# Performance work log

Measured on AMD Instinct MI355X. Metric: run time of the kernel, lower is better.

The kernel has to match this reference:

```python
import jax, jax.numpy as jnp
import numpy as np

EMBED = 768
HEADS = 12
HEAD_DIM = EMBED // HEADS
HIDDEN = 4 * EMBED


def layer_norm(x, gamma, beta, eps=1e-5):
    mu = jnp.mean(x, axis=-1, keepdims=True)
    var = jnp.var(x, axis=-1, keepdims=True)
    return (x - mu) * jax.lax.rsqrt(var + eps) * gamma + beta


def setup_inputs() -> dict:
    key = jax.random.key(0)
    ks = jax.random.split(key, 10)
    B, N, C = 64, 577, EMBED
    s_in = 1.0 / np.sqrt(C)
    s_hid = 1.0 / np.sqrt(HIDDEN)
    return {
        "x": jax.random.normal(ks[0], (B, N, C), jnp.float32),
        "ln1_g": jnp.ones((C,), jnp.float32),
        "ln1_b": jnp.zeros((C,), jnp.float32),
        "w_qkv": jax.random.normal(ks[1], (C, 3 * C), jnp.float32) * s_in,  # no bias (qkv_bias=False)
        "w_proj": jax.random.normal(ks[2], (C, C), jnp.float32) * s_in,
        "b_proj": jnp.zeros((C,), jnp.float32),
        "ln2_g": jnp.ones((C,), jnp.float32),
        "ln2_b": jnp.zeros((C,), jnp.float32),
        "w_fc1": jax.random.normal(ks[3], (C, HIDDEN), jnp.float32) * s_in,
        "b_fc1": jnp.zeros((HIDDEN,), jnp.float32),
        "w_fc2": jax.random.normal(ks[4], (HIDDEN, C), jnp.float32) * s_hid,
        "b_fc2": jnp.zeros((C,), jnp.float32),
    }


def reference(x, ln1_g, ln1_b, w_qkv, w_proj, b_proj, ln2_g, ln2_b, w_fc1, b_fc1, w_fc2, b_fc2):
    B, N, C = x.shape
    # --- attention branch (pre-norm) ---
    h = layer_norm(x, ln1_g, ln1_b)
    qkv = (h @ w_qkv).reshape(B, N, 3, HEADS, HEAD_DIM)
    q = jnp.transpose(qkv[:, :, 0], (0, 2, 1, 3))  # [B,H,N,D]
    k = jnp.transpose(qkv[:, :, 1], (0, 2, 1, 3))
    v = jnp.transpose(qkv[:, :, 2], (0, 2, 1, 3))
    scale = HEAD_DIM ** -0.5
    att = jax.nn.softmax(jnp.einsum("bhnd,bhmd->bhnm", q, k) * scale, axis=-1)
    o = jnp.einsum("bhnm,bhmd->bhnd", att, v)
    o = jnp.transpose(o, (0, 2, 1, 3)).reshape(B, N, C)
    x = x + (o @ w_proj + b_proj)
    # --- MLP branch (pre-norm) ---
    h = layer_norm(x, ln2_g, ln2_b)
    h = jax.nn.gelu(h @ w_fc1 + b_fc1, approximate=False)
    x = x + (h @ w_fc2 + b_fc2)
    return x
```

## Files before the change

kernel.cpp:

```cpp
#include <hip/hip_runtime.h>
#include <hip/hip_bf16.h>
#include <math.h>

using bf16 = __hip_bfloat16;
typedef __attribute__((ext_vector_type(8))) short short8;
typedef __attribute__((ext_vector_type(4))) float f32x4;

#define NSEQ   577
#define NBATCH 64
#define NTOK   36928
#define MPAD   37120
#define NHEADS 12
#define HDIM   64
#define NP     640
#define CEMB   768
#define CHID   3072
#define NBH    (NBATCH*NHEADS)

__device__ __forceinline__ bf16 f2bf(float v){ return __float2bfloat16(v); }

__device__ __forceinline__ float gelu_f(float x) {
    float x3 = x * x * x;
    float y = 1.5957691216057308f * (x + 0.044715f * x3);
    float e = __expf(y);
    float t = 1.0f - 2.0f / (e + 1.0f);
    return 0.5f * x * (1.0f + t);
}

#define GLOAD_LDS16(gaddr, laddr) \
  __builtin_amdgcn_global_load_lds((__attribute__((address_space(1))) const void*)(gaddr), \
                                   (__attribute__((address_space(3))) void*)(laddr), 16, 0, 0)

__global__ __launch_bounds__(256) void transpose_w(const float* __restrict__ src,
                                                   bf16* __restrict__ dst, int R, int C) {
    long idx = (long)blockIdx.x * 256 + threadIdx.x;
    long total = (long)R * C;
    if (idx < total) {
        int r = (int)(idx / C);
        int c = (int)(idx - (long)r * C);
        dst[(long)c * R + r] = f2bf(src[idx]);
    }
}

__global__ __launch_bounds__(256) void ln_kernel(const float* __restrict__ x,
                                                 const float* __restrict__ gamma,
                                                 const float* __restrict__ beta,
                                                 bf16* __restrict__ out) {
    int row = blockIdx.x;
    const float* xr = x + (size_t)row * CEMB;
    int tid = threadIdx.x;
    float v0 = xr[tid], v1 = xr[tid + 256], v2 = xr[tid + 512];
    float s = v0 + v1 + v2;
    #pragma unroll
    for (int o = 32; o > 0; o >>= 1) s += __shfl_down(s, o);
    __shared__ float red[4];
    if ((tid & 63) == 0) red[tid >> 6] = s;
    __syncthreads();
    float mean = (red[0] + red[1] + red[2] + red[3]) * (1.0f / CEMB);
    float d0 = v0 - mean, d1 = v1 - mean, d2 = v2 - mean;
    float q = d0*d0 + d1*d1 + d2*d2;
    #pragma unroll
    for (int o = 32; o > 0; o >>= 1) q += __shfl_down(q, o);
    __shared__ float red2[4];
    if ((tid & 63) == 0) red2[tid >> 6] = q;
    __syncthreads();
    float var = (red2[0] + red2[1] + red2[2] + red2[3]) * (1.0f / CEMB);
    float rs = rsqrtf(var + 1e-5f);
    bf16* orow = out + (size_t)row * CEMB;
    orow[tid]       = f2bf(d0 * rs * gamma[tid]       + beta[tid]);
    orow[tid + 256] = f2bf(d1 * rs * gamma[tid + 256] + beta[tid + 256]);
    orow[tid + 512] = f2bf(d2 * rs * gamma[tid + 512] + beta[tid + 512]);
}

__global__ __launch_bounds__(256) void flash_attn(const bf16* __restrict__ qg,
                                                  const bf16* __restrict__ kg,
                                                  const bf16* __restrict__ vtg,
                                                  bf16* __restrict__ og) {
    const int tid = threadIdx.x, lane = tid & 63, w = tid >> 6;
    const int fr = lane & 15, fh = lane >> 4;
    const int bh = blockIdx.y;
    const int q0 = blockIdx.x * 128;
    const int wr = w * 32;

    __shared__ bf16 Ks[2][64 * 64];
    __shared__ bf16 Vs[2][64 * 64];
    __shared__ bf16 Ps[128 * 64];

    const bf16* qb = qg  + (size_t)bh * NP * HDIM;
    const bf16* kb = kg  + (size_t)bh * NP * HDIM;
    const bf16* vb = vtg + (size_t)bh * HDIM * NP;

    const int swz  = (fr & 7) << 3;
    const int scol = (((lane & 7) ^ (lane >> 3)) << 3);
    const int srow = lane >> 3;

    short8 qa[2][2];
    #pragma unroll
    for (int mi = 0; mi < 2; mi++)
        #pragma unroll
        for (int ks = 0; ks < 2; ks++)
            qa[mi][ks] = *reinterpret_cast<const short8*>(
                qb + (size_t)(q0 + wr + mi * 16 + fr) * HDIM + ks * 32 + fh * 8);
    #pragma unroll
    for (int mi = 0; mi < 2; mi++)
        #pragma unroll
        for (int ks = 0; ks < 2; ks++)
            asm volatile("" : "+v"(qa[mi][ks]));

    f32x4 od[2][4] = {};
    float m_run[2][4], l_run[2][4];
    #pragma unroll
    for (int mi = 0; mi < 2; mi++)
        #pragma unroll
        for (int r = 0; r < 4; r++) { m_run[mi][r] = -1e30f; l_run[mi][r] = 0.f; }

    auto stageKV = [&](int buf, int kb0) {
        GLOAD_LDS16(kb + (size_t)(kb0 + w * 8 + srow) * HDIM + scol,      Ks[buf] + w * 512);
        GLOAD_LDS16(kb + (size_t)(kb0 + 32 + w * 8 + srow) * HDIM + scol, Ks[buf] + 2048 + w * 512);
        GLOAD_LDS16(vb + (size_t)(w * 8 + srow) * NP + kb0 + scol,        Vs[buf] + w * 512);
        GLOAD_LDS16(vb + (size_t)(32 + w * 8 + srow) * NP + kb0 + scol,   Vs[buf] + 2048 + w * 512);
    };

    auto tileBody = [&](int buf, int kb0) {
        f32x4 sacc[2][4] = {};
        short8 kf[4][2];
        #pragma unroll
        for (int n = 0; n < 4; n++)
            #pragma unroll
            for (int ks = 0; ks < 2; ks++)
                kf[n][ks] = *reinterpret_cast<const short8*>(
                    &Ks[buf][(n * 16 + fr) * 64 + ((ks * 32 + fh * 8) ^ swz)]);
        __builtin_amdgcn_s_setprio(1);
        #pragma unroll
        for (int mi = 0; mi < 2; mi++)
            #pragma unroll
            for (int n = 0; n < 4; n++)
                #pragma unroll
                for (int ks = 0; ks < 2; ks++)
                    sacc[mi][n] = __builtin_amdgcn_mfma_f32_16x16x32_bf16(qa[mi][ks], kf[n][ks], sacc[mi][n], 0, 0, 0);
        __builtin_amdgcn_s_setprio(0);

        #pragma unroll
        for (int mi = 0; mi < 2; mi++) {
            float sv[4][4];
            float tm[4] = {-1e30f, -1e30f, -1e30f, -1e30f};
            #pragma unroll
            for (int n = 0; n < 4; n++) {
                int col = kb0 + n * 16 + fr;
                bool valid = col < NSEQ;
                #pragma unroll
                for (int r = 0; r < 4; r++) {
                    float s = sacc[mi][n][r];
                    sv[n][r] = valid ? s : -1e30f;
                    tm[r] = fmaxf(tm[r], sv[n][r]);
                }
            }
            #pragma unroll
            for (int r = 0; r < 4; r++) {
                #pragma unroll
                for (int o = 1; o < 16; o <<= 1) tm[r] = fmaxf(tm[r], __shfl_xor(tm[r], o));
                float mo = m_run[mi][r];
                if (tm[r] - mo > 8.f) {
                    float sc = __expf(mo - tm[r]);
                    mo = tm[r];
                    m_run[mi][r] = mo;
                    l_run[mi][r] *= sc;
                    #pragma unroll
                    for (int n2 = 0; n2 < 4; n2++) od[mi][n2][r] *= sc;
                }
                float ps = 0.f;
                #pragma unroll
                for (int n = 0; n < 4; n++) {
                    float e = __expf(sv[n][r] - mo);
                    sv[n][r] = e; ps += e;
                }
                #pragma unroll
                for (int o = 1; o < 16; o <<= 1) ps += __shfl_xor(ps, o);
                l_run[mi][r] += ps;
            }
            #pragma unroll
            for (int n = 0; n < 4; n++)
                #pragma unroll
                for (int r = 0; r < 4; r++)
                    Ps[(wr + mi * 16 + fh * 4 + r) * 64 +
                       ((n * 16 + fr) ^ (((fh * 4 + r) & 7) << 3))] = f2bf(sv[n][r]);
        }
        asm volatile("s_waitcnt lgkmcnt(0)" ::: "memory");
        __builtin_amdgcn_sched_barrier(0);

        short8 pa[2][2], vf[4][2];
        #pragma unroll
        for (int mi = 0; mi < 2; mi++)
            #pragma unroll
            for (int ks = 0; ks < 2; ks++)
                pa[mi][ks] = *reinterpret_cast<const short8*>(
                    &Ps[(wr + mi * 16 + fr) * 64 + ((ks * 32 + fh * 8) ^ swz)]);
        #pragma unroll
        for (int n2 = 0; n2 < 4; n2++)
            #pragma unroll
            for (int ks = 0; ks < 2; ks++)
                vf[n2][ks] = *reinterpret_cast<const short8*>(
                    &Vs[buf][(n2 * 16 + fr) * 64 + ((ks * 32 + fh * 8) ^ swz)]);
        __builtin_amdgcn_s_setprio(1);
        #pragma unroll
        for (int mi = 0; mi < 2; mi++)
            #pragma unroll
            for (int n2 = 0; n2 < 4; n2++)
                #pragma unroll
                for (int ks = 0; ks < 2; ks++)
                    od[mi][n2] = __builtin_amdgcn_mfma_f32_16x16x32_bf16(pa[mi][ks], vf[n2][ks], od[mi][n2], 0, 0, 0);
        __builtin_amdgcn_s_setprio(0);
    };

    stageKV(0, 0);
    stageKV(1, 64);
    for (int t = 0; t < 9; ++t) {
        asm volatile("s_waitcnt vmcnt(4)" ::: "memory");
        __builtin_amdgcn_s_barrier();
        tileBody(t & 1, t * 64);
        asm volatile("s_waitcnt lgkmcnt(0)" ::: "memory");
        __builtin_amdgcn_s_barrier();
        if (t + 2 < 10) stageKV(t & 1, (t + 2) * 64);
    }
    asm volatile("s_waitcnt vmcnt(0)" ::: "memory");
    __builtin_amdgcn_s_barrier();
    tileBody(1, 9 * 64);

    const int b = bh / NHEADS, hh = bh - b * NHEADS;
    #pragma unroll
    for (int mi = 0; mi < 2; mi++)
        #pragma unroll
        for (int r = 0; r < 4; r++) {
            int qrow = q0 + wr + mi * 16 + fh * 4 + r;
            if (qrow < NSEQ) {
                float inv = 1.f / l_run[mi][r];
                #pragma unroll
                for (int n2 = 0; n2 < 4; n2++)
                    og[((size_t)(b * NSEQ + qrow)) * CEMB + hh * HDIM + n2 * 16 + fr] =
                        f2bf(od[mi][n2][r] * inv);
            }
        }
}

#define MODE_QKV  1
#define MODE_PROJ 3
#define MODE_FC1  4
#define MODE_FC2  5

struct GemmParams {
    const bf16* A;
    const bf16* Bt;
    int M, N, K;
    int Mreal;
    float* Cf;
    bf16* Cb;
    const float* bias;
    const float* resid;
    bf16* qb; bf16* kb; bf16* vtb;
};

template<int MODE>
__global__ __launch_bounds__(512, 2) void gemm256(GemmParams p) {
    __shared__ bf16 AsBuf[2][256 * 64];
    __shared__ bf16 BsBuf[2][256 * 64];
    const int tid  = threadIdx.x;
    const int lane = tid & 63;
    const int w    = tid >> 6;

    const int gx = gridDim.x, gy = gridDim.y;
    const int nwg = gx * gy;
    const int orig = blockIdx.y * gx + blockIdx.x;
    const int q8 = nwg >> 3, r8 = nwg & 7;
    const int xcd = orig & 7, oid = orig >> 3;
    const int lin2 = ((xcd < r8) ? xcd * (q8 + 1) : r8 * (q8 + 1) + (xcd - r8) * q8) + oid;
    const int bm = (lin2 / gy) * 256;
    const int bn = (lin2 % gy) * 256;

    const int Kd = p.K;
    const int wm = w >> 2, wn = w & 3;
    const int wr = wm * 128, wc = wn * 64;
    const int fr = lane & 15;
    const int fk = (lane >> 4) * 8;
    const int swz = (fr & 7) << 3;

    const int sr = w * 8 + (lane >> 3);
    const int scol = (((lane & 7) ^ (lane >> 3)) << 3);
    const bf16* aS[4]; const bf16* bS[4];
    #pragma unroll
    for (int s = 0; s < 4; s++) {
        aS[s] = p.A  + (size_t)(bm + s * 64 + sr) * Kd + scol;
        bS[s] = p.Bt + (size_t)(bn + s * 64 + sr) * Kd + scol;
    }

    f32x4 acc[8][4] = {};

    auto stage = [&](bf16* Ad, bf16* Bd) {
        #pragma unroll
        for (int s = 0; s < 4; s++) {
            GLOAD_LDS16(aS[s], Ad + (size_t)(s * 8 + w) * 512);
            GLOAD_LDS16(bS[s], Bd + (size_t)(s * 8 + w) * 512);
            aS[s] += 64; bS[s] += 64;
        }
    };
    auto compute = [&](const bf16* Ad, const bf16* Bd) {
        #pragma unroll
        for (int ks = 0; ks < 2; ks++) {
            short8 b[4];
            #pragma unroll
            for (int n = 0; n < 4; n++)
                b[n] = *reinterpret_cast<const short8*>(
                    &Bd[(wc + n * 16 + fr) * 64 + ((ks * 32 + fk) ^ swz)]);
            #pragma unroll
            for (int m = 0; m < 8; m++) {
                short8 a = *reinterpret_cast<const short8*>(
                    &Ad[(wr + m * 16 + fr) * 64 + ((ks * 32 + fk) ^ swz)]);
                #pragma unroll
                for (int n = 0; n < 4; n++)
                    acc[m][n] = __builtin_amdgcn_mfma_f32_16x16x32_bf16(a, b[n], acc[m][n], 0, 0, 0);
            }
        }
    };

    const int T = Kd >> 6;
    stage(AsBuf[0], BsBuf[0]);
    stage(AsBuf[1], BsBuf[1]);
    for (int t = 0; t < T - 1; ++t) {
        asm volatile("s_waitcnt vmcnt(8)" ::: "memory");
        __builtin_amdgcn_s_barrier();
        compute(AsBuf[t & 1], BsBuf[t & 1]);
        asm volatile("s_waitcnt lgkmcnt(0)" ::: "memory");
        __builtin_amdgcn_s_barrier();
        if (t + 2 < T) stage(AsBuf[t & 1], BsBuf[t & 1]);
    }
    asm volatile("s_waitcnt vmcnt(0)" ::: "memory");
    __builtin_amdgcn_s_barrier();
    compute(AsBuf[(T - 1) & 1], BsBuf[(T - 1) & 1]);

    const int fq = (lane >> 4) * 4;
    const int colw = bn + wc;

    if (MODE == MODE_QKV) {
        const int which = colw / CEMB;
        const int hh = (colw - which * CEMB) >> 6;
        const float scl = (which == 0) ? 0.125f : 1.0f;
        #pragma unroll
        for (int m = 0; m < 8; m++)
        #pragma unroll
        for (int r = 0; r < 4; r++) {
            int row = bm + wr + m * 16 + fq + r;
            if (row < p.Mreal) {
                int b2 = row / NSEQ;
                int n2 = row - b2 * NSEQ;
                size_t bh = (size_t)b2 * NHEADS + hh;
                if (which == 0) {
                    bf16* dst = p.qb + (bh * NP + n2) * HDIM + fr;
                    #pragma unroll
                    for (int n = 0; n < 4; n++) dst[n * 16] = f2bf(acc[m][n][r] * scl);
                } else if (which == 1) {
                    bf16* dst = p.kb + (bh * NP + n2) * HDIM + fr;
                    #pragma unroll
                    for (int n = 0; n < 4; n++) dst[n * 16] = f2bf(acc[m][n][r]);
                } else {
                    bf16* dst = p.vtb + (bh * HDIM + fr) * NP + n2;
                    #pragma unroll
                    for (int n = 0; n < 4; n++) dst[(size_t)n * 16 * NP] = f2bf(acc[m][n][r]);
                }
            }
        }
    } else if (MODE == MODE_FC1) {
        const float* bp = p.bias + colw + fr;
        float bb[4];
        #pragma unroll
        for (int n = 0; n < 4; n++) bb[n] = bp[n * 16];
        #pragma unroll
        for (int m = 0; m < 8; m++)
        #pragma unroll
        for (int r = 0; r < 4; r++) {
            int row = bm + wr + m * 16 + fq + r;
            if (row < p.Mreal) {
                bf16* crow = p.Cb + (size_t)row * p.N + colw + fr;
                #pragma unroll
                for (int n = 0; n < 4; n++)
                    crow[n * 16] = f2bf(gelu_f(acc[m][n][r] + bb[n]));
            }
        }
    } else {
        const float* bp = p.bias + colw + fr;
        float bb[4];
        #pragma unroll
        for (int n = 0; n < 4; n++) bb[n] = bp[n * 16];
        #pragma unroll
        for (int m = 0; m < 8; m++)
        #pragma unroll
        for (int r = 0; r < 4; r++) {
            int row = bm + wr + m * 16 + fq + r;
            if (row < p.Mreal) {
                float* crow = p.Cf + (size_t)row * p.N + colw + fr;
                const float* rrow = p.resid + (size_t)row * p.N + colw + fr;
                #pragma unroll
                for (int n = 0; n < 4; n++)
                    crow[n * 16] = acc[m][n][r] + bb[n] + rrow[n * 16];
            }
        }
    }
}

extern "C" void kernel_launch(void* const* d_in, const int* in_sizes, int n_in,
                              void* d_out, int out_size, void* d_ws, size_t ws_size,
                              hipStream_t stream) {
    const float* x      = (const float*)d_in[0];
    const float* ln1_g  = (const float*)d_in[1];
    const float* ln1_b  = (const float*)d_in[2];
    const float* w_qkv  = (const float*)d_in[3];
    const float* w_proj = (const float*)d_in[4];
    const float* b_proj = (const float*)d_in[5];
    const float* ln2_g  = (const float*)d_in[6];
    const float* ln2_b  = (const float*)d_in[7];
    const float* w_fc1  = (const float*)d_in[8];
    const float* b_fc1  = (const float*)d_in[9];
    const float* w_fc2  = (const float*)d_in[10];
    const float* b_fc2  = (const float*)d_in[11];
    float* out = (float*)d_out;

    char* ws = (char*)d_ws;
    auto al = [](size_t b){ return (b + 255) & ~(size_t)255; };
    size_t off = 0;
    auto take = [&](size_t b)->char* { char* p = ws + off; off += al(b); return p; };

    bf16* wqkvT  = (bf16*)take((size_t)2304 * 768 * 2);
    bf16* wprojT = (bf16*)take((size_t)768 * 768 * 2);
    bf16* wfc1T  = (bf16*)take((size_t)3072 * 768 * 2);
    bf16* wfc2T  = (bf16*)take((size_t)768 * 3072 * 2);
    bf16* h      = (bf16*)take((size_t)MPAD * CEMB * 2);
    bf16* o      = (bf16*)take((size_t)MPAD * CEMB * 2);
    size_t fixedEnd = off;

    const size_t qkvB = (size_t)NBH * NP * HDIM * 2;
    bf16* q_c  = (bf16*)(ws + fixedEnd);
    bf16* k_c  = (bf16*)(ws + fixedEnd + qkvB);
    bf16* vT_c = (bf16*)(ws + fixedEnd + 2 * qkvB);
    bf16* g_c  = (bf16*)(ws + fixedEnd);

    transpose_w<<<(768 * 2304 + 255) / 256, 256, 0, stream>>>(w_qkv, wqkvT, 768, 2304);
    transpose_w<<<(768 * 768 + 255) / 256, 256, 0, stream>>>(w_proj, wprojT, 768, 768);
    transpose_w<<<(768 * 3072 + 255) / 256, 256, 0, stream>>>(w_fc1, wfc1T, 768, 3072);
    transpose_w<<<(3072 * 768 + 255) / 256, 256, 0, stream>>>(w_fc2, wfc2T, 3072, 768);

    ln_kernel<<<NTOK, 256, 0, stream>>>(x, ln1_g, ln1_b, h);

    {
        GemmParams p{};
        p.A = h; p.Bt = wqkvT;
        p.M = MPAD; p.N = 3 * CEMB; p.K = CEMB; p.Mreal = NTOK;
        p.qb = q_c; p.kb = k_c; p.vtb = vT_c;
        gemm256<MODE_QKV><<<dim3(MPAD / 256, 3 * CEMB / 256), 512, 0, stream>>>(p);
    }

    flash_attn<<<dim3(NP / 128, NBH), 256, 0, stream>>>(q_c, k_c, vT_c, o);

    {
        GemmParams p{};
        p.A = o; p.Bt = wprojT;
        p.M = MPAD; p.N = CEMB; p.K = CEMB; p.Mreal = NTOK;
        p.Cf = out; p.bias = b_proj; p.resid = x;
        gemm256<MODE_PROJ><<<dim3(MPAD / 256, CEMB / 256), 512, 0, stream>>>(p);
    }

    ln_kernel<<<NTOK, 256, 0, stream>>>(out, ln2_g, ln2_b, h);

    {
        GemmParams p{};
        p.A = h; p.Bt = wfc1T;
        p.M = MPAD; p.N = CHID; p.K = CEMB; p.Mreal = NTOK;
        p.Cb = g_c; p.bias = b_fc1;
        gemm256<MODE_FC1><<<dim3(MPAD / 256, CHID / 256), 512, 0, stream>>>(p);
    }

    {
        GemmParams p{};
        p.A = g_c; p.Bt = wfc2T;
        p.M = MPAD; p.N = CEMB; p.K = CHID; p.Mreal = NTOK;
        p.Cf = out; p.bias = b_fc2; p.resid = out;
        gemm256<MODE_FC2><<<dim3(MPAD / 256, CEMB / 256), 512, 0, stream>>>(p);
    }
}
```

Baseline: 1.405 ms.

## Transpose QK^T MFMA for per-lane softmax rows and simplify GEMM pipeline

The attention kernel swaps the MFMA operands so each lane holds scores for one query row across several keys. Row max and sum then need only two cross-lane shuffles instead of four-step reductions per row, and running stats shrink to one value per lane. P is written to LDS as packed 8-byte stores. Separately, the GEMM main loop moves from a two-stage prefetch with explicit vmcnt waits to a simpler stage-then-compute loop with __syncthreads, which may reduce load/compute overlap.

```diff
diff --git a/kernel.cpp b/kernel.cpp
--- a/kernel.cpp
+++ b/kernel.cpp
@@ -108,11 +108,8 @@
             asm volatile("" : "+v"(qa[mi][ks]));
 
     f32x4 od[2][4] = {};
-    float m_run[2][4], l_run[2][4];
-    #pragma unroll
-    for (int mi = 0; mi < 2; mi++)
-        #pragma unroll
-        for (int r = 0; r < 4; r++) { m_run[mi][r] = -1e30f; l_run[mi][r] = 0.f; }
+    float m_run[2] = {-1e30f, -1e30f};
+    float l_run[2] = {0.f, 0.f};
 
     auto stageKV = [&](int buf, int kb0) {
         GLOAD_LDS16(kb + (size_t)(kb0 + w * 8 + srow) * HDIM + scol,      Ks[buf] + w * 512);
@@ -137,53 +134,63 @@
             for (int n = 0; n < 4; n++)
                 #pragma unroll
                 for (int ks = 0; ks < 2; ks++)
-                    sacc[mi][n] = __builtin_amdgcn_mfma_f32_16x16x32_bf16(qa[mi][ks], kf[n][ks], sacc[mi][n], 0, 0, 0);
+                    sacc[mi][n] = __builtin_amdgcn_mfma_f32_16x16x32_bf16(kf[n][ks], qa[mi][ks], sacc[mi][n], 0, 0, 0);
         __builtin_amdgcn_s_setprio(0);
 
         #pragma unroll
         for (int mi = 0; mi < 2; mi++) {
             float sv[4][4];
-            float tm[4] = {-1e30f, -1e30f, -1e30f, -1e30f};
-            #pragma unroll
-            for (int n = 0; n < 4; n++) {
-                int col = kb0 + n * 16 + fr;
-                bool valid = col < NSEQ;
+            float tm = -1e30f;
+            #pragma unroll
+            for (int n = 0; n < 4; n++)
                 #pragma unroll
                 for (int r = 0; r < 4; r++) {
+                    int key = kb0 + n * 16 + fh * 4 + r;
                     float s = sacc[mi][n][r];
-                    sv[n][r] = valid ? s : -1e30f;
-                    tm[r] = fmaxf(tm[r], sv[n][r]);
+                    sv[n][r] = (key < NSEQ) ? s : -1e30f;
+                    tm = fmaxf(tm, sv[n][r]);
                 }
-            }
-            #pragma unroll
-            for (int r = 0; r < 4; r++) {
-                #pragma unroll
-                for (int o = 1; o < 16; o <<= 1) tm[r] = fmaxf(tm[r], __shfl_xor(tm[r], o));
-                float mo = m_run[mi][r];
-                if (tm[r] - mo > 8.f) {
-                    float sc = __expf(mo - tm[r]);
-                    mo = tm[r];
-                    m_run[mi][r] = mo;
-                    l_run[mi][r] *= sc;
+            tm = fmaxf(tm, __shfl_xor(tm, 16));
+            tm = fmaxf(tm, __shfl_xor(tm, 32));
+            float mo = m_run[mi];
+            if (__any(tm - mo > 8.f)) {
+                float mn = fmaxf(mo, tm);
+                float sc = __expf(mo - mn);
+                m_run[mi] = mn;
+                l_run[mi] *= sc;
+                #pragma unroll
+                for (int r = 0; r < 4; r++) {
+                    float s2 = __shfl(sc, fh * 4 + r);
                     #pragma unroll
-                    for (int n2 = 0; n2 < 4; n2++) od[mi][n2][r] *= sc;
+                    for (int n2 = 0; n2 < 4; n2++) od[mi][n2][r] *= s2;
                 }
-                float ps = 0.f;
-                #pragma unroll
-                for (int n = 0; n < 4; n++) {
+                mo = mn;
+            }
+            float ps = 0.f;
+            #pragma unroll
+            for (int n = 0; n < 4; n++)
+                #pragma unroll
+                for (int r = 0; r < 4; r++) {
                     float e = __expf(sv[n][r] - mo);
                     sv[n][r] = e; ps += e;
                 }
-                #pragma unroll
-                for (int o = 1; o < 16; o <<= 1) ps += __shfl_xor(ps, o);
-                l_run[mi][r] += ps;
-            }
-            #pragma unroll
-            for (int n = 0; n < 4; n++)
-                #pragma unroll
-                for (int r = 0; r < 4; r++)
-                    Ps[(wr + mi * 16 + fh * 4 + r) * 64 +
-                       ((n * 16 + fr) ^ (((fh * 4 + r) & 7) << 3))] = f2bf(sv[n][r]);
+            ps += __shfl_xor(ps, 16);
+            ps += __shfl_xor(ps, 32);
+            l_run[mi] += ps;
+            const int q = wr + mi * 16 + fr;
+            char* prow = (char*)(Ps + q * 64);
+            #pragma unroll
+            for (int n = 0; n < 4; n++) {
+                bf16 b0 = f2bf(sv[n][0]), b1 = f2bf(sv[n][1]);
+                bf16 b2 = f2bf(sv[n][2]), b3 = f2bf(sv[n][3]);
+                unsigned int lo = (unsigned int)*(unsigned short*)&b0 |
+                                  ((unsigned int)*(unsigned short*)&b1 << 16);
+                unsigned int hi = (unsigned int)*(unsigned short*)&b2 |
+                                  ((unsigned int)*(unsigned short*)&b3 << 16);
+                int chunk = (2 * n + (fh >> 1)) ^ (fr & 7);
+                uint2 pk; pk.x = lo; pk.y = hi;
+                *reinterpret_cast<uint2*>(prow + (chunk << 4) + ((fh & 1) << 3)) = pk;
+            }
         }
         asm volatile("s_waitcnt lgkmcnt(0)" ::: "memory");
         __builtin_amdgcn_sched_barrier(0);
@@ -231,9 +238,10 @@
     for (int mi = 0; mi < 2; mi++)
         #pragma unroll
         for (int r = 0; r < 4; r++) {
+            float lv = __shfl(l_run[mi], fh * 4 + r);
             int qrow = q0 + wr + mi * 16 + fh * 4 + r;
             if (qrow < NSEQ) {
-                float inv = 1.f / l_run[mi][r];
+                float inv = 1.f / lv;
                 #pragma unroll
                 for (int n2 = 0; n2 < 4; n2++)
                     og[((size_t)(b * NSEQ + qrow)) * CEMB + hh * HDIM + n2 * 16 + fr] =
@@ -323,17 +331,12 @@
 
     const int T = Kd >> 6;
     stage(AsBuf[0], BsBuf[0]);
-    stage(AsBuf[1], BsBuf[1]);
-    for (int t = 0; t < T - 1; ++t) {
-        asm volatile("s_waitcnt vmcnt(8)" ::: "memory");
-        __builtin_amdgcn_s_barrier();
-        compute(AsBuf[t & 1], BsBuf[t & 1]);
-        asm volatile("s_waitcnt lgkmcnt(0)" ::: "memory");
-        __builtin_amdgcn_s_barrier();
-        if (t + 2 < T) stage(AsBuf[t & 1], BsBuf[t & 1]);
-    }
-    asm volatile("s_waitcnt vmcnt(0)" ::: "memory");
-    __builtin_amdgcn_s_barrier();
+    __syncthreads();
+    for (int t = 1; t < T; ++t) {
+        stage(AsBuf[t & 1], BsBuf[t & 1]);
+        compute(AsBuf[(t - 1) & 1], BsBuf[(t - 1) & 1]);
+        __syncthreads();
+    }
     compute(AsBuf[(T - 1) & 1], BsBuf[(T - 1) & 1]);
 
     const int fq = (lane >> 4) * 4;
```

Result: faster. 1.302 ms (-7.3%).
